# Kernel tuning notes

Measured on AMD Instinct MI355X. Metric: run time of the kernel, lower is better.

## Reference

```python
import jax, jax.numpy as jnp
import numpy as np


def quantize(weights):
    # per-output-channel threshold alpha = mean |w| over in_features
    alpha = jnp.mean(jnp.abs(weights), axis=1, keepdims=True)  # (out, 1)
    return jnp.where(weights > alpha, 1.0,
                     jnp.where(weights < -alpha, -1.0, 0.0)).astype(weights.dtype)


def setup_inputs() -> dict:
    key = jax.random.key(0)
    k1, k2 = jax.random.split(key)
    B, S, DIN, DOUT = 4, 2048, 4096, 4096
    x = jax.random.normal(k1, (B, S, DIN), dtype=jnp.float32)
    weight = jax.random.normal(k2, (DOUT, DIN), dtype=jnp.float32)
    scale = jnp.ones((DOUT, 1), dtype=jnp.float32)
    bias = jnp.zeros((DOUT,), dtype=jnp.float32)
    return {"x": x, "weight": weight, "scale": scale, "bias": bias}


def reference(x, weight, scale, bias):
    # training-mode path with straight-through estimator
    q = quantize(weight)
    qw = jax.lax.stop_gradient(q) + weight - jax.lax.stop_gradient(weight)
    scaled_weight = qw * scale  # (out, in)
    # F.linear: x @ W^T + b
    out = jnp.einsum('bsi,oi->bso', x, scaled_weight) + bias
    return out
```

## Files before the change

### kernel.cpp

```cpp
#include <hip/hip_runtime.h>
#include <hip/hip_bf16.h>
#include <stdint.h>

#define DIN   4096
#define DOUT  4096
#define MTOT  8192

#define BK    64
#define NKT   (DIN / BK)

typedef int i32x4 __attribute__((ext_vector_type(4)));

__device__ __forceinline__ void glds16(const void* g, void* l) {
  __builtin_amdgcn_global_load_lds(
      (__attribute__((address_space(1))) void*)g,
      (__attribute__((address_space(3))) void*)l, 16, 0, 0);
}

__global__ __launch_bounds__(256) void quant_w(const float* __restrict__ W,
                                               int8_t* __restrict__ QW) {
  const int row = blockIdx.x;
  const int t = threadIdx.x;
  const float* wr = W + (size_t)row * DIN;

  float4 v[4];
  double s = 0.0;
#pragma unroll
  for (int j = 0; j < 4; ++j) {
    v[j] = reinterpret_cast<const float4*>(wr)[j * 256 + t];
    s += (double)fabsf(v[j].x) + (double)fabsf(v[j].y) +
         (double)fabsf(v[j].z) + (double)fabsf(v[j].w);
  }
#pragma unroll
  for (int off = 32; off > 0; off >>= 1) s += __shfl_down(s, off, 64);

  __shared__ double ssum[4];
  __shared__ float salpha;
  if ((t & 63) == 0) ssum[t >> 6] = s;
  __syncthreads();
  if (t == 0) salpha = (float)((ssum[0] + ssum[1] + ssum[2] + ssum[3]) / (double)DIN);
  __syncthreads();
  const float alpha = salpha;

  int* qo = reinterpret_cast<int*>(QW + (size_t)row * DIN);
#pragma unroll
  for (int j = 0; j < 4; ++j) {
    int q0 = v[j].x > alpha ? 1 : (v[j].x < -alpha ? -1 : 0);
    int q1 = v[j].y > alpha ? 1 : (v[j].y < -alpha ? -1 : 0);
    int q2 = v[j].z > alpha ? 1 : (v[j].z < -alpha ? -1 : 0);
    int q3 = v[j].w > alpha ? 1 : (v[j].w < -alpha ? -1 : 0);
    qo[j * 256 + t] =
        (q0 & 0xff) | ((q1 & 0xff) << 8) | ((q2 & 0xff) << 16) | ((q3 & 0xff) << 24);
  }
}

__global__ __launch_bounds__(256) void quant_x(const float* __restrict__ X,
                                               int8_t* __restrict__ XQ,
                                               float* __restrict__ XS) {
  const int row = blockIdx.x;
  const int t = threadIdx.x;
  const float* xr = X + (size_t)row * DIN;

  float4 v[4];
  float mx = 0.f;
#pragma unroll
  for (int j = 0; j < 4; ++j) {
    v[j] = reinterpret_cast<const float4*>(xr)[j * 256 + t];
    mx = fmaxf(mx, fmaxf(fmaxf(fabsf(v[j].x), fabsf(v[j].y)),
                         fmaxf(fabsf(v[j].z), fabsf(v[j].w))));
  }
#pragma unroll
  for (int off = 32; off > 0; off >>= 1) mx = fmaxf(mx, __shfl_down(mx, off, 64));

  __shared__ float smax[4];
  __shared__ float sinv, ssc;
  if ((t & 63) == 0) smax[t >> 6] = mx;
  __syncthreads();
  if (t == 0) {
    float rm = fmaxf(fmaxf(smax[0], smax[1]), fmaxf(smax[2], smax[3]));
    sinv = rm > 0.f ? 127.f / rm : 0.f;
    ssc  = rm > 0.f ? rm / 127.f : 0.f;
  }
  __syncthreads();
  const float inv = sinv;
  if (t == 0) XS[row] = ssc;

  int* qo = reinterpret_cast<int*>(XQ + (size_t)row * DIN);
#pragma unroll
  for (int j = 0; j < 4; ++j) {
    int q0 = (int)rintf(v[j].x * inv);
    int q1 = (int)rintf(v[j].y * inv);
    int q2 = (int)rintf(v[j].z * inv);
    int q3 = (int)rintf(v[j].w * inv);
    qo[j * 256 + t] =
        (q0 & 0xff) | ((q1 & 0xff) << 8) | ((q2 & 0xff) << 16) | ((q3 & 0xff) << 24);
  }
}

__global__ __launch_bounds__(1024, 4) void gemm256_i8(
    const int8_t* __restrict__ XQ, const int8_t* __restrict__ QW,
    const float* __restrict__ XS, const float* __restrict__ scale,
    const float* __restrict__ bias, float* __restrict__ out) {
  __shared__ int8_t As[2][16384];
  __shared__ int8_t Bs[2][16384];

  const int t = threadIdx.x;
  const int lane = t & 63;
  const int wid = t >> 6;
  const int wr = wid >> 2, wc = wid & 3;
  const int m0 = blockIdx.x * 256;
  const int n0 = blockIdx.y * 256;

  const int8_t* ag = XQ + (size_t)m0 * DIN;
  const int8_t* bg = QW + (size_t)n0 * DIN;

  i32x4 acc[4][4] = {};
  i32x4 a[4], b[4];

  const int r = lane & 15, kq = lane >> 4;
  const int srow = t >> 2;
  const int scol = ((t & 3) ^ ((srow >> 1) & 3)) * 16;

#define ISSUE_T(Tt_, isb_) do {                                                 \
    const int T_ = (Tt_);                                                       \
    if (T_ < NKT) {                                                             \
      const int bf_ = T_ & 1;                                                   \
      const int8_t* gb_ = (isb_) ? bg : ag;                                     \
      int8_t* lb_ = (isb_) ? &Bs[bf_][0] : &As[bf_][0];                         \
      glds16(gb_ + (size_t)srow * DIN + T_ * 64 + scol, lb_ + t * 16);          \
    }                                                                           \
  } while (0)

#define READA(buf_) do {                                                        \
    _Pragma("unroll")                                                           \
    for (int mi = 0; mi < 4; ++mi) {                                            \
      const int row_ = wr * 64 + mi * 16 + r;                                   \
      a[mi] = *reinterpret_cast<const i32x4*>(                                  \
          &As[buf_][row_ * 64 + (kq ^ ((row_ >> 1) & 3)) * 16]);                \
    }                                                                           \
  } while (0)

#define READB(buf_) do {                                                        \
    _Pragma("unroll")                                                           \
    for (int ni = 0; ni < 4; ++ni) {                                            \
      const int row_ = wc * 64 + ni * 16 + r;                                   \
      b[ni] = *reinterpret_cast<const i32x4*>(                                  \
          &Bs[buf_][row_ * 64 + (kq ^ ((row_ >> 1) & 3)) * 16]);                \
    }                                                                           \
  } while (0)

#define MMA8(nh_) do {                                                          \
    __builtin_amdgcn_s_setprio(1);                                              \
    _Pragma("unroll")                                                           \
    for (int mi = 0; mi < 4; ++mi) {                                            \
      _Pragma("unroll")                                                         \
      for (int ni = 0; ni < 2; ++ni) {                                          \
        acc[mi][(nh_) * 2 + ni] =                                               \
            __builtin_amdgcn_mfma_i32_16x16x64_i8(                              \
                a[mi], b[(nh_) * 2 + ni], acc[mi][(nh_) * 2 + ni], 0, 0, 0);    \
      }                                                                         \
    }                                                                           \
    __builtin_amdgcn_s_setprio(0);                                              \
  } while (0)

#define BAR() __builtin_amdgcn_s_barrier()

#define TILE(T_, buf_) do {                                                     \
             \
    READA(buf_);                                                                \
    READB(buf_);                                                                \
    ISSUE_T((T_) + 1, 0);                                                       \
    MMA8(0);                                                                    \
    BAR();                                                                      \
                   \
    ISSUE_T((T_) + 2, 1);                                                       \
    MMA8(1);                                                                    \
    if ((T_) < NKT - 2)                                                         \
      asm volatile("s_waitcnt vmcnt(1)" ::: "memory");                          \
    else                                                                        \
      asm volatile("s_waitcnt vmcnt(0)" ::: "memory");                          \
    BAR();                                                                      \
  } while (0)

  ISSUE_T(0, 0); ISSUE_T(0, 1); ISSUE_T(1, 1);
  asm volatile("s_waitcnt vmcnt(1)" ::: "memory");
  __builtin_amdgcn_s_barrier();

  for (int T = 0; T < NKT; T += 2) {
    TILE(T, 0);
    TILE(T + 1, 1);
  }

  const int q4 = lane >> 4;
#pragma unroll
  for (int ni = 0; ni < 4; ++ni) {
    const int col = n0 + wc * 64 + ni * 16 + r;
    const float sc = scale[col];
    const float bs = bias[col];
#pragma unroll
    for (int mi = 0; mi < 4; ++mi) {
      const int row = m0 + wr * 64 + mi * 16 + q4 * 4;
#pragma unroll
      for (int e = 0; e < 4; ++e) {
        const float xs = XS[row + e];
        out[(size_t)(row + e) * DOUT + col] =
            (float)acc[mi][ni][e] * (xs * sc) + bs;
      }
    }
  }
#undef ISSUE_T
#undef READA
#undef READB
#undef MMA8
#undef BAR
#undef TILE
}

extern "C" void kernel_launch(void* const* d_in, const int* in_sizes, int n_in,
                              void* d_out, int out_size, void* d_ws, size_t ws_size,
                              hipStream_t stream) {
  const float* X     = (const float*)d_in[0];
  const float* W     = (const float*)d_in[1];
  const float* scale = (const float*)d_in[2];
  const float* bias  = (const float*)d_in[3];
  float* out = (float*)d_out;

  int8_t* QW = (int8_t*)d_ws;
  int8_t* XQ = (int8_t*)d_ws + (size_t)DOUT * DIN;
  float*  XS = (float*)((int8_t*)d_ws + (size_t)DOUT * DIN + (size_t)MTOT * DIN);

  quant_w<<<DOUT, 256, 0, stream>>>(W, QW);
  quant_x<<<MTOT, 256, 0, stream>>>(X, XQ, XS);
  dim3 grid(MTOT / 256, DOUT / 256);
  gemm256_i8<<<grid, 1024, 0, stream>>>(XQ, QW, XS, scale, bias, out);
}
```

Baseline: 200.3 us.

## Quad-buffer A tiles in LDS to prefetch two k-steps ahead

Expands the A-operand LDS staging from two to four buffers and issues A global-to-LDS loads two k-tiles ahead. B stays double-buffered but its loads are also issued two tiles ahead into the buffer just consumed. An explicit lgkmcnt(0) wait is added before the first barrier. The vmcnt thresholds change to allow more loads in flight, and the main loop is unrolled by four. The aim is to hide global load latency better, at the cost of more LDS (96KB) and an extra wait.

```diff
diff --git a/kernel.cpp b/kernel.cpp
--- a/kernel.cpp
+++ b/kernel.cpp
@@ -101,7 +101,7 @@
     const int8_t* __restrict__ XQ, const int8_t* __restrict__ QW,
     const float* __restrict__ XS, const float* __restrict__ scale,
     const float* __restrict__ bias, float* __restrict__ out) {
-  __shared__ int8_t As[2][16384];
+  __shared__ int8_t As[4][16384];
   __shared__ int8_t Bs[2][16384];
 
   const int t = threadIdx.x;
@@ -121,31 +121,33 @@
   const int srow = t >> 2;
   const int scol = ((t & 3) ^ ((srow >> 1) & 3)) * 16;
 
-#define ISSUE_T(Tt_, isb_) do {                                                 \
+#define ISSUE_A(Tt_, ab_) do {                                                  \
     const int T_ = (Tt_);                                                       \
-    if (T_ < NKT) {                                                             \
-      const int bf_ = T_ & 1;                                                   \
-      const int8_t* gb_ = (isb_) ? bg : ag;                                     \
-      int8_t* lb_ = (isb_) ? &Bs[bf_][0] : &As[bf_][0];                         \
-      glds16(gb_ + (size_t)srow * DIN + T_ * 64 + scol, lb_ + t * 16);          \
-    }                                                                           \
-  } while (0)
-
-#define READA(buf_) do {                                                        \
+    if (T_ < NKT)                                                               \
+      glds16(ag + (size_t)srow * DIN + T_ * 64 + scol, &As[ab_][0] + t * 16);   \
+  } while (0)
+
+#define ISSUE_B(Tt_, bb_) do {                                                  \
+    const int T_ = (Tt_);                                                       \
+    if (T_ < NKT)                                                               \
+      glds16(bg + (size_t)srow * DIN + T_ * 64 + scol, &Bs[bb_][0] + t * 16);   \
+  } while (0)
+
+#define READA(ab_) do {                                                         \
     _Pragma("unroll")                                                           \
     for (int mi = 0; mi < 4; ++mi) {                                            \
       const int row_ = wr * 64 + mi * 16 + r;                                   \
       a[mi] = *reinterpret_cast<const i32x4*>(                                  \
-          &As[buf_][row_ * 64 + (kq ^ ((row_ >> 1) & 3)) * 16]);                \
+          &As[ab_][row_ * 64 + (kq ^ ((row_ >> 1) & 3)) * 16]);                 \
     }                                                                           \
   } while (0)
 
-#define READB(buf_) do {                                                        \
+#define READB(bb_) do {                                                         \
     _Pragma("unroll")                                                           \
     for (int ni = 0; ni < 4; ++ni) {                                            \
       const int row_ = wc * 64 + ni * 16 + r;                                   \
       b[ni] = *reinterpret_cast<const i32x4*>(                                  \
-          &Bs[buf_][row_ * 64 + (kq ^ ((row_ >> 1) & 3)) * 16]);                \
+          &Bs[bb_][row_ * 64 + (kq ^ ((row_ >> 1) & 3)) * 16]);                 \
     }                                                                           \
   } while (0)
 
@@ -164,31 +166,35 @@
   } while (0)
 
 #define BAR() __builtin_amdgcn_s_barrier()
-
-#define TILE(T_, buf_) do {                                                     \
-             \
-    READA(buf_);                                                                \
-    READB(buf_);                                                                \
-    ISSUE_T((T_) + 1, 0);                                                       \
+#define LGKM0() asm volatile("s_waitcnt lgkmcnt(0)" ::: "memory")
+
+#define TILE(T_, ab_, bb_) do {                                                 \
+           \
+    READA(ab_);                                                                 \
+    READB(bb_);                                                                 \
+    ISSUE_A((T_) + 2, ((T_) + 2) & 3);                                          \
     MMA8(0);                                                                    \
+    LGKM0();     \
     BAR();                                                                      \
-                   \
-    ISSUE_T((T_) + 2, 1);                                                       \
+         \
+    ISSUE_B((T_) + 2, bb_);                                                     \
     MMA8(1);                                                                    \
     if ((T_) < NKT - 2)                                                         \
-      asm volatile("s_waitcnt vmcnt(1)" ::: "memory");                          \
+      asm volatile("s_waitcnt vmcnt(2)" ::: "memory");                          \
     else                                                                        \
       asm volatile("s_waitcnt vmcnt(0)" ::: "memory");                          \
     BAR();                                                                      \
   } while (0)
 
-  ISSUE_T(0, 0); ISSUE_T(0, 1); ISSUE_T(1, 1);
-  asm volatile("s_waitcnt vmcnt(1)" ::: "memory");
+  ISSUE_A(0, 0); ISSUE_B(0, 0); ISSUE_A(1, 1); ISSUE_B(1, 1);
+  asm volatile("s_waitcnt vmcnt(2)" ::: "memory");
   __builtin_amdgcn_s_barrier();
 
-  for (int T = 0; T < NKT; T += 2) {
-    TILE(T, 0);
-    TILE(T + 1, 1);
+  for (int T = 0; T < NKT; T += 4) {
+    TILE(T,     (T) & 3,     0);
+    TILE(T + 1, (T + 1) & 3, 1);
+    TILE(T + 2, (T + 2) & 3, 0);
+    TILE(T + 3, (T + 3) & 3, 1);
   }
 
   const int q4 = lane >> 4;
@@ -208,11 +214,13 @@
       }
     }
   }
-#undef ISSUE_T
+#undef ISSUE_A
+#undef ISSUE_B
 #undef READA
 #undef READB
 #undef MMA8
 #undef BAR
+#undef LGKM0
 #undef TILE
 }
 
```

New measurement: 266.2 us. 1.33x slower.
